# Optimization experiments

Hardware: AMD Instinct MI355X
Metric: run time of the kernel (lower is better)

The kernel has to match this reference:

```python
import jax, jax.numpy as jnp
import numpy as np

B, N, D = 64, 4096, 512
ATT = 128


def setup_inputs() -> dict:
    key = jax.random.key(0)
    ks = jax.random.split(key, 7)
    s = lambda fan_in: 1.0 / np.sqrt(fan_in)
    return {
        "v_I": jax.random.normal(ks[0], (B, N, D), dtype=jnp.float32),
        "v_Q": jax.random.normal(ks[1], (B, D), dtype=jnp.float32),
        "W_I": jax.random.normal(ks[2], (D, ATT), dtype=jnp.float32) * s(D),
        "W_Q": jax.random.normal(ks[3], (D, ATT), dtype=jnp.float32) * s(D),
        "b_Q": jnp.zeros((ATT,), dtype=jnp.float32),
        "W_p": jax.random.normal(ks[4], (ATT, 1), dtype=jnp.float32) * s(ATT),
        "b_p": jnp.zeros((1,), dtype=jnp.float32),
    }


def reference(v_I, v_Q, W_I, W_Q, b_Q, W_p, b_p):
    # v_I: [B, N, D], v_Q: [B, D]
    v_I_att = jnp.tanh(jnp.einsum("bnd,da->bna", v_I, W_I))          # [B, N, A]
    v_Q_att = jnp.tanh(v_Q @ W_Q + b_Q)[:, None, :]                  # [B, 1, A]
    h_A = jnp.tanh(v_I_att + v_Q_att)                                # [B, N, A]
    # dropout is identity in inference/reference mode
    p_I = (jnp.einsum("bna,ao->bno", h_A, W_p) + b_p)[..., 0]        # [B, N]
    p_I_output = jax.nn.softmax(p_I, axis=-1)                        # [B, N]
    v_att = jnp.einsum("bn,bnd->bd", p_I_output, v_I)                # [B, D]
    u = v_att + v_Q                                                  # [B, D]
    return (p_I_output, u)
```

## Files before the change

kernel.cpp:

```cpp
#include <hip/hip_runtime.h>
#include <cstdint>
#include <cstddef>

#define B_ 64
#define N_ 4096
#define D_ 512
#define A_ 128

typedef unsigned short u16;
typedef __attribute__((ext_vector_type(8))) short bf16x8;
typedef __attribute__((ext_vector_type(4))) float f32x4;

__device__ __forceinline__ u16 cvt_bf16(float x) {
    unsigned u = __float_as_uint(x);
    return (u16)((u + 0x7FFFu + ((u >> 16) & 1u)) >> 16);
}
__device__ __forceinline__ unsigned pack2_bf16(float a, float b) {
    unsigned ua = __float_as_uint(a), ub = __float_as_uint(b);
    unsigned ra = (ua + 0x7FFFu + ((ua >> 16) & 1u)) >> 16;
    unsigned rb = (ub + 0x7FFFu + ((ub >> 16) & 1u)) >> 16;
    return ra | (rb << 16);
}
__device__ __forceinline__ float fast_tanh(float x) {
    float ax = fabsf(x);
    float e  = __expf(-2.0f * ax);
    float r  = __fdividef(1.0f - e, 1.0f + e);
    return x < 0.0f ? -r : r;
}

__global__ void k_prep(const float* __restrict__ WI, const float* __restrict__ vQ,
                       const float* __restrict__ WQ, const float* __restrict__ bQ,
                       u16* __restrict__ Wbf, float* __restrict__ qatt,
                       float* __restrict__ sums, float* __restrict__ u) {
    const int blk = blockIdx.x, t = threadIdx.x;
    if (blk < 64) {
        #pragma unroll
        for (int i = 0; i < 2; ++i) {
            int item = blk * 256 + i * 128 + t;
            int a  = item & 127;
            int d0 = (item >> 7) << 2;
            ushort4 r;
            r.x = cvt_bf16(WI[(d0 + 0) * A_ + a]);
            r.y = cvt_bf16(WI[(d0 + 1) * A_ + a]);
            r.z = cvt_bf16(WI[(d0 + 2) * A_ + a]);
            r.w = cvt_bf16(WI[(d0 + 3) * A_ + a]);
            *(ushort4*)&Wbf[a * D_ + d0] = r;
        }
    } else {
        const int b = blk - 64;
        __shared__ float sq[D_];
        for (int d = t; d < D_; d += 128) sq[d] = vQ[b * D_ + d];
        __syncthreads();
        float acc = bQ[t];
        #pragma unroll 8
        for (int d = 0; d < D_; ++d) acc += sq[d] * WQ[d * A_ + t];
        qatt[b * A_ + t] = fast_tanh(acc);
        float4 vq4 = *(const float4*)(vQ + b * D_ + t * 4);
        *(float4*)(u + b * D_ + t * 4) = vq4;
        if (t == 0) sums[b] = 0.0f;
    }
}

__global__ void __launch_bounds__(256)
k_gemm(const float* __restrict__ vI, const u16* __restrict__ Wbf,
       const float* __restrict__ qatt, const float* __restrict__ Wp,
       float* __restrict__ w_out, float* __restrict__ sums) {
    const int b  = blockIdx.y;
    const int n0 = blockIdx.x * 128;
    const int t    = threadIdx.x;
    const int lane = t & 63, wave = t >> 6;
    const int l15  = lane & 15, quad = lane >> 4;

    f32x4 acc[2][8];
    #pragma unroll
    for (int mt = 0; mt < 2; ++mt)
        #pragma unroll
        for (int nt = 0; nt < 8; ++nt)
            acc[mt][nt] = (f32x4){0.f, 0.f, 0.f, 0.f};

    const float* a0p = vI + (size_t)(b * N_ + n0 + wave * 32 + l15) * D_ + quad * 8;
    const float* a1p = a0p + 16 * D_;
    const u16* bbase = Wbf + (size_t)l15 * D_ + quad * 8;

    #pragma unroll 2
    for (int kk = 0; kk < 16; ++kk) {
        const int ko = kk * 32;
        float4 a0a = *(const float4*)(a0p + ko);
        float4 a0b = *(const float4*)(a0p + ko + 4);
        float4 a1a = *(const float4*)(a1p + ko);
        float4 a1b = *(const float4*)(a1p + ko + 4);
        bf16x8 bfr[8];
        #pragma unroll
        for (int nt = 0; nt < 8; ++nt)
            bfr[nt] = *(const bf16x8*)(bbase + nt * 16 * D_ + ko);
        union { bf16x8 v; unsigned u[4]; } c0, c1;
        c0.u[0] = pack2_bf16(a0a.x, a0a.y);
        c0.u[1] = pack2_bf16(a0a.z, a0a.w);
        c0.u[2] = pack2_bf16(a0b.x, a0b.y);
        c0.u[3] = pack2_bf16(a0b.z, a0b.w);
        c1.u[0] = pack2_bf16(a1a.x, a1a.y);
        c1.u[1] = pack2_bf16(a1a.z, a1a.w);
        c1.u[2] = pack2_bf16(a1b.x, a1b.y);
        c1.u[3] = pack2_bf16(a1b.z, a1b.w);
        bf16x8 af[2] = { c0.v, c1.v };
        #pragma unroll
        for (int mt = 0; mt < 2; ++mt)
            #pragma unroll
            for (int nt = 0; nt < 8; ++nt)
                acc[mt][nt] = __builtin_amdgcn_mfma_f32_16x16x32_bf16(
                    af[mt], bfr[nt], acc[mt][nt], 0, 0, 0);
    }

    float qa_v[8], wp_v[8];
    #pragma unroll
    for (int nt = 0; nt < 8; ++nt) {
        int a = nt * 16 + l15;
        qa_v[nt] = qatt[b * A_ + a];
        wp_v[nt] = Wp[a];
    }
    float lsum = 0.f;
    #pragma unroll
    for (int mt = 0; mt < 2; ++mt) {
        #pragma unroll
        for (int r = 0; r < 4; ++r) {
            float s = 0.f;
            #pragma unroll
            for (int nt = 0; nt < 8; ++nt) {
                float t1 = fast_tanh(acc[mt][nt][r]);
                float h  = fast_tanh(t1 + qa_v[nt]);
                s += h * wp_v[nt];
            }
            s += __shfl_xor(s, 1, 16);
            s += __shfl_xor(s, 2, 16);
            s += __shfl_xor(s, 4, 16);
            s += __shfl_xor(s, 8, 16);
            float we = __expf(s);
            lsum += we;
            if (l15 == 0)
                w_out[(size_t)b * N_ + n0 + wave * 32 + mt * 16 + quad * 4 + r] = we;
        }
    }
    lsum += __shfl_xor(lsum, 16, 64);
    lsum += __shfl_xor(lsum, 32, 64);
    __shared__ float wred[4];
    if (lane == 0) wred[wave] = lsum;
    __syncthreads();
    if (t == 0) atomicAdd(sums + b, wred[0] + wred[1] + wred[2] + wred[3]);
}

__global__ void __launch_bounds__(256)
k_wsum(const float* __restrict__ vI, const float* __restrict__ w,
       const float* __restrict__ sums, float* __restrict__ p_out,
       float* __restrict__ u) {
    const int b  = blockIdx.y;
    const int n0 = blockIdx.x * 256;
    const int t  = threadIdx.x;
    const float inv = 1.0f / sums[b];
    __shared__ float sp[256];
    float pv = w[(size_t)b * N_ + n0 + t] * inv;
    sp[t] = pv;
    p_out[(size_t)b * N_ + n0 + t] = pv;
    __syncthreads();
    const int rr = t >> 7;
    const int c  = t & 127;
    const float4* base = (const float4*)(vI + (size_t)(b * N_ + n0 + rr) * D_) + c;
    float a0 = 0.f, a1 = 0.f, a2 = 0.f, a3 = 0.f;
    #pragma unroll 8
    for (int n = 0; n < 256; n += 2) {
        float4 x = base[n * 128];
        float wn = sp[n + rr];
        a0 += wn * x.x; a1 += wn * x.y; a2 += wn * x.z; a3 += wn * x.w;
    }
    float* ub = u + b * D_ + c * 4;
    atomicAdd(ub + 0, a0);
    atomicAdd(ub + 1, a1);
    atomicAdd(ub + 2, a2);
    atomicAdd(ub + 3, a3);
}

extern "C" void kernel_launch(void* const* d_in, const int* in_sizes, int n_in,
                              void* d_out, int out_size, void* d_ws, size_t ws_size,
                              hipStream_t stream) {
    const float* vI = (const float*)d_in[0];
    const float* vQ = (const float*)d_in[1];
    const float* WI = (const float*)d_in[2];
    const float* WQ = (const float*)d_in[3];
    const float* bQ = (const float*)d_in[4];
    const float* Wp = (const float*)d_in[5];

    float* out_p = (float*)d_out;
    float* out_u = out_p + (size_t)B_ * N_;

    char* ws = (char*)d_ws;
    u16*   Wbf  = (u16*)ws;
    float* qatt = (float*)(ws + 131072);
    float* sums = (float*)(ws + 131072 + 32768);
    float* wbuf = (float*)(ws + 131072 + 32768 + 1024);

    k_prep<<<128, 128, 0, stream>>>(WI, vQ, WQ, bQ, Wbf, qatt, sums, out_u);
    k_gemm<<<dim3(N_ / 128, B_), 256, 0, stream>>>(vI, Wbf, qatt, Wp, wbuf, sums);
    k_wsum<<<dim3(N_ / 256, B_), 256, 0, stream>>>(vI, wbuf, sums, out_p, out_u);
}
```

Baseline: 873.2 us.

## Fuse weighted sum into GEMM kernel using unnormalized softmax weights and finalize

```diff
diff --git a/kernel.cpp b/kernel.cpp
--- a/kernel.cpp
+++ b/kernel.cpp
@@ -31,7 +31,7 @@
 __global__ void k_prep(const float* __restrict__ WI, const float* __restrict__ vQ,
                        const float* __restrict__ WQ, const float* __restrict__ bQ,
                        u16* __restrict__ Wbf, float* __restrict__ qatt,
-                       float* __restrict__ sums, float* __restrict__ u) {
+                       float* __restrict__ sums, float* __restrict__ u_raw) {
     const int blk = blockIdx.x, t = threadIdx.x;
     if (blk < 64) {
         #pragma unroll
@@ -55,22 +55,26 @@
         #pragma unroll 8
         for (int d = 0; d < D_; ++d) acc += sq[d] * WQ[d * A_ + t];
         qatt[b * A_ + t] = fast_tanh(acc);
-        float4 vq4 = *(const float4*)(vQ + b * D_ + t * 4);
-        *(float4*)(u + b * D_ + t * 4) = vq4;
+        float4 z = {0.f, 0.f, 0.f, 0.f};
+        *(float4*)(u_raw + b * D_ + t * 4) = z;
         if (t == 0) sums[b] = 0.0f;
     }
 }
 
 __global__ void __launch_bounds__(256)
-k_gemm(const float* __restrict__ vI, const u16* __restrict__ Wbf,
-       const float* __restrict__ qatt, const float* __restrict__ Wp,
-       float* __restrict__ w_out, float* __restrict__ sums) {
+k_fused(const float* __restrict__ vI, const u16* __restrict__ Wbf,
+        const float* __restrict__ qatt, const float* __restrict__ Wp,
+        float* __restrict__ wbuf, float* __restrict__ sums,
+        float* __restrict__ u_raw) {
     const int b  = blockIdx.y;
     const int n0 = blockIdx.x * 128;
     const int t    = threadIdx.x;
     const int lane = t & 63, wave = t >> 6;
     const int l15  = lane & 15, quad = lane >> 4;
 
+    __shared__ float sw[128];
+    __shared__ float wred[4];
+
     f32x4 acc[2][8];
     #pragma unroll
     for (int mt = 0; mt < 2; ++mt)
@@ -82,26 +86,33 @@
     const float* a1p = a0p + 16 * D_;
     const u16* bbase = Wbf + (size_t)l15 * D_ + quad * 8;
 
-    #pragma unroll 2
+    float4 c0a = *(const float4*)(a0p);
+    float4 c0b = *(const float4*)(a0p + 4);
+    float4 c1a = *(const float4*)(a1p);
+    float4 c1b = *(const float4*)(a1p + 4);
+    #pragma unroll
     for (int kk = 0; kk < 16; ++kk) {
-        const int ko = kk * 32;
-        float4 a0a = *(const float4*)(a0p + ko);
-        float4 a0b = *(const float4*)(a0p + ko + 4);
-        float4 a1a = *(const float4*)(a1p + ko);
-        float4 a1b = *(const float4*)(a1p + ko + 4);
+        float4 n0a, n0b, n1a, n1b;
+        if (kk < 15) {
+            const int ko = (kk + 1) * 32;
+            n0a = *(const float4*)(a0p + ko);
+            n0b = *(const float4*)(a0p + ko + 4);
+            n1a = *(const float4*)(a1p + ko);
+            n1b = *(const float4*)(a1p + ko + 4);
+        }
         bf16x8 bfr[8];
         #pragma unroll
         for (int nt = 0; nt < 8; ++nt)
-            bfr[nt] = *(const bf16x8*)(bbase + nt * 16 * D_ + ko);
+            bfr[nt] = *(const bf16x8*)(bbase + nt * 16 * D_ + kk * 32);
         union { bf16x8 v; unsigned u[4]; } c0, c1;
-        c0.u[0] = pack2_bf16(a0a.x, a0a.y);
-        c0.u[1] = pack2_bf16(a0a.z, a0a.w);
-        c0.u[2] = pack2_bf16(a0b.x, a0b.y);
-        c0.u[3] = pack2_bf16(a0b.z, a0b.w);
-        c1.u[0] = pack2_bf16(a1a.x, a1a.y);
-        c1.u[1] = pack2_bf16(a1a.z, a1a.w);
-        c1.u[2] = pack2_bf16(a1b.x, a1b.y);
-        c1.u[3] = pack2_bf16(a1b.z, a1b.w);
+        c0.u[0] = pack2_bf16(c0a.x, c0a.y);
+        c0.u[1] = pack2_bf16(c0a.z, c0a.w);
+        c0.u[2] = pack2_bf16(c0b.x, c0b.y);
+        c0.u[3] = pack2_bf16(c0b.z, c0b.w);
+        c1.u[0] = pack2_bf16(c1a.x, c1a.y);
+        c1.u[1] = pack2_bf16(c1a.z, c1a.w);
+        c1.u[2] = pack2_bf16(c1b.x, c1b.y);
+        c1.u[3] = pack2_bf16(c1b.z, c1b.w);
         bf16x8 af[2] = { c0.v, c1.v };
         #pragma unroll
         for (int mt = 0; mt < 2; ++mt)
@@ -109,6 +120,7 @@
             for (int nt = 0; nt < 8; ++nt)
                 acc[mt][nt] = __builtin_amdgcn_mfma_f32_16x16x32_bf16(
                     af[mt], bfr[nt], acc[mt][nt], 0, 0, 0);
+        c0a = n0a; c0b = n0b; c1a = n1a; c1b = n1b;
     }
 
     float qa_v[8], wp_v[8];
@@ -136,46 +148,55 @@
             s += __shfl_xor(s, 8, 16);
             float we = __expf(s);
             lsum += we;
-            if (l15 == 0)
-                w_out[(size_t)b * N_ + n0 + wave * 32 + mt * 16 + quad * 4 + r] = we;
+            if (l15 == 0) {
+                int rloc = wave * 32 + mt * 16 + quad * 4 + r;
+                wbuf[(size_t)b * N_ + n0 + rloc] = we;
+                sw[rloc] = we;
+            }
         }
     }
     lsum += __shfl_xor(lsum, 16, 64);
     lsum += __shfl_xor(lsum, 32, 64);
-    __shared__ float wred[4];
     if (lane == 0) wred[wave] = lsum;
     __syncthreads();
     if (t == 0) atomicAdd(sums + b, wred[0] + wred[1] + wred[2] + wred[3]);
-}
-
-__global__ void __launch_bounds__(256)
-k_wsum(const float* __restrict__ vI, const float* __restrict__ w,
-       const float* __restrict__ sums, float* __restrict__ p_out,
-       float* __restrict__ u) {
-    const int b  = blockIdx.y;
-    const int n0 = blockIdx.x * 256;
-    const int t  = threadIdx.x;
-    const float inv = 1.0f / sums[b];
-    __shared__ float sp[256];
-    float pv = w[(size_t)b * N_ + n0 + t] * inv;
-    sp[t] = pv;
-    p_out[(size_t)b * N_ + n0 + t] = pv;
-    __syncthreads();
+
     const int rr = t >> 7;
     const int c  = t & 127;
     const float4* base = (const float4*)(vI + (size_t)(b * N_ + n0 + rr) * D_) + c;
     float a0 = 0.f, a1 = 0.f, a2 = 0.f, a3 = 0.f;
     #pragma unroll 8
-    for (int n = 0; n < 256; n += 2) {
+    for (int n = 0; n < 128; n += 2) {
         float4 x = base[n * 128];
-        float wn = sp[n + rr];
+        float wn = sw[n + rr];
         a0 += wn * x.x; a1 += wn * x.y; a2 += wn * x.z; a3 += wn * x.w;
     }
-    float* ub = u + b * D_ + c * 4;
+    float* ub = u_raw + b * D_ + c * 4;
     atomicAdd(ub + 0, a0);
     atomicAdd(ub + 1, a1);
     atomicAdd(ub + 2, a2);
     atomicAdd(ub + 3, a3);
+}
+
+__global__ void __launch_bounds__(256)
+k_fin(const float* __restrict__ wbuf, const float* __restrict__ sums,
+      const float* __restrict__ u_raw, const float* __restrict__ vQ,
+      float* __restrict__ p_out, float* __restrict__ u_out) {
+    const int b = blockIdx.x, t = threadIdx.x;
+    const float inv = 1.0f / sums[b];
+    #pragma unroll
+    for (int i = 0; i < 4; ++i) {
+        float4 x = *(const float4*)(wbuf + (size_t)b * N_ + i * 1024 + t * 4);
+        float4 y = { x.x * inv, x.y * inv, x.z * inv, x.w * inv };
+        *(float4*)(p_out + (size_t)b * N_ + i * 1024 + t * 4) = y;
+    }
+    if (t < 128) {
+        float4 ur = *(const float4*)(u_raw + b * D_ + t * 4);
+        float4 vq = *(const float4*)(vQ + b * D_ + t * 4);
+        float4 o  = { ur.x * inv + vq.x, ur.y * inv + vq.y,
+                      ur.z * inv + vq.z, ur.w * inv + vq.w };
+        *(float4*)(u_out + b * D_ + t * 4) = o;
+    }
 }
 
 extern "C" void kernel_launch(void* const* d_in, const int* in_sizes, int n_in,
@@ -192,12 +213,14 @@
     float* out_u = out_p + (size_t)B_ * N_;
 
     char* ws = (char*)d_ws;
-    u16*   Wbf  = (u16*)ws;
-    float* qatt = (float*)(ws + 131072);
-    float* sums = (float*)(ws + 131072 + 32768);
-    float* wbuf = (float*)(ws + 131072 + 32768 + 1024);
-
-    k_prep<<<128, 128, 0, stream>>>(WI, vQ, WQ, bQ, Wbf, qatt, sums, out_u);
-    k_gemm<<<dim3(N_ / 128, B_), 256, 0, stream>>>(vI, Wbf, qatt, Wp, wbuf, sums);
-    k_wsum<<<dim3(N_ / 256, B_), 256, 0, stream>>>(vI, wbuf, sums, out_p, out_u);
-}
+    u16*   Wbf   = (u16*)ws;
+    float* qatt  = (float*)(ws + 131072);
+    float* sums  = (float*)(ws + 163840);
+    float* u_raw = (float*)(ws + 164864);
+    float* wbuf  = (float*)(ws + 295936);
+
+    k_prep<<<128, 128, 0, stream>>>(WI, vQ, WQ, bQ, Wbf, qatt, sums, u_raw);
+    k_fused<<<dim3(N_ / 128, B_), 256, 0, stream>>>(vI, Wbf, qatt, Wp,
+                                                    wbuf, sums, u_raw);
+    k_fin<<<B_, 256, 0, stream>>>(wbuf, sums, u_raw, vQ, out_p, out_u);
+}
```

After: 833.6 us. 1.05x faster.
